# Kernel tuning notes

Hardware: AMD Instinct MI355X
Metric: run time of the kernel (lower is better)

The kernel has to match this reference:

```python
import jax, jax.numpy as jnp
import numpy as np

N = 50000          # nodes
E = 1_600_000      # edges (avg degree 32)
IN_CH = 256
HID = 256          # 2 * out_channels
OUT_CH = 128


def setup_inputs() -> dict:
    key = jax.random.key(0)
    k = jax.random.split(key, 5)
    x = jax.random.normal(k[0], (N, IN_CH), dtype=jnp.float32)
    edge_index = jax.random.randint(k[1], (2, E), 0, N, dtype=jnp.int64)
    W1 = jax.random.normal(k[2], (IN_CH, HID), dtype=jnp.float32) * 0.05
    b1 = jnp.zeros((HID,), dtype=jnp.float32)
    W2 = jax.random.normal(k[3], (HID, OUT_CH), dtype=jnp.float32) * 0.05
    b2 = jnp.zeros((OUT_CH,), dtype=jnp.float32)
    return {"x": x, "edge_index": edge_index, "W1": W1, "b1": b1, "W2": W2, "b2": b2}


def _gcn_conv(x, src, dst, deg_inv_sqrt, W, b, n_nodes):
    # GCNConv: linear transform, then normalized sum-aggregation over edges
    # (edge list already includes self-loops; deg_inv_sqrt precomputed).
    h = x @ W                                   # [N, F_out]
    norm = deg_inv_sqrt[src] * deg_inv_sqrt[dst]  # [E+N]
    msg = h[src] * norm[:, None]                # gather + scale
    out = jax.ops.segment_sum(msg, dst, num_segments=n_nodes)  # scatter-add
    return out + b


def reference(x, edge_index, W1, b1, W2, b2):
    n = x.shape[0]
    loop = jnp.arange(n, dtype=edge_index.dtype)
    src = jnp.concatenate([edge_index[0], loop])   # with self-loops
    dst = jnp.concatenate([edge_index[1], loop])
    # symmetric degree normalization (edge weight 1, deg over targets)
    deg = jax.ops.segment_sum(jnp.ones_like(dst, dtype=x.dtype), dst, num_segments=n)
    deg_inv_sqrt = jnp.where(deg > 0, jax.lax.rsqrt(deg), 0.0)

    z = _gcn_conv(x, src, dst, deg_inv_sqrt, W1, b1, n)
    z = jax.nn.relu(z)
    z = _gcn_conv(z, src, dst, deg_inv_sqrt, W2, b2, n)

    # decode: gather endpoint embeddings of original edges, dot product
    value = jnp.sum(z[edge_index[0]] * z[edge_index[1]], axis=-1)  # [E]
    return value.reshape(-1)
```

## Files before the change

### kernel.cpp

```cpp
#include <hip/hip_runtime.h>

#define WS_ALIGN(x) (((x) + 255) & ~(size_t)255)

typedef float f4v __attribute__((ext_vector_type(4)));
__device__ inline void nt_store4(float* p, float4 v) {
  __builtin_nontemporal_store(*(f4v*)&v, (f4v*)p);
}

__global__ void k_pack_count(const int* __restrict__ src, const int* __restrict__ dst, int E,
                             unsigned int* __restrict__ packed, int* __restrict__ deg) {
  int e = blockIdx.x * blockDim.x + threadIdx.x;
  if (e < E) {
    int s = src[e];
    int d = dst[e];
    packed[e] = (unsigned int)s | ((unsigned int)d << 16);
    atomicAdd(&deg[d], 1);
  }
}

__global__ void k_dis(const int* __restrict__ deg, float* __restrict__ dis, int N) {
  int i = blockIdx.x * blockDim.x + threadIdx.x;
  if (i < N) dis[i] = rsqrtf((float)(deg[i] + 1));
}

__global__ __launch_bounds__(1024) void k_scan(const int* __restrict__ deg,
                                               int* __restrict__ rowptr,
                                               int* __restrict__ cursor,
                                               int N, int Etot) {
  __shared__ int wsum[16];
  __shared__ int s_carry;
  int tid = threadIdx.x, lane = tid & 63, w = tid >> 6;
  if (tid == 0) { s_carry = 0; rowptr[N] = Etot; }
  __syncthreads();
  for (int base = 0; base < N; base += 4096) {
    int i0 = base + tid * 4;
    int v[4];
    #pragma unroll
    for (int u = 0; u < 4; ++u) {
      int i = i0 + u;
      v[u] = (i < N) ? deg[i] : 0;
    }
    int tsum = v[0] + v[1] + v[2] + v[3];
    int sc = tsum;
    #pragma unroll
    for (int off = 1; off < 64; off <<= 1) {
      int t = __shfl_up(sc, off);
      if (lane >= off) sc += t;
    }
    if (lane == 63) wsum[w] = sc;
    __syncthreads();
    if (w == 0 && lane < 16) {
      int xx = wsum[lane];
      #pragma unroll
      for (int off = 1; off < 16; off <<= 1) {
        int t = __shfl_up(xx, off);
        if (lane >= off) xx += t;
      }
      wsum[lane] = xx;
    }
    __syncthreads();
    int woff = (w == 0) ? 0 : wsum[w - 1];
    int excl = s_carry + woff + (sc - tsum);
    #pragma unroll
    for (int u = 0; u < 4; ++u) {
      int i = i0 + u;
      if (i < N) { rowptr[i] = excl; cursor[i] = excl; }
      excl += v[u];
    }
    __syncthreads();
    if (tid == 0) s_carry += wsum[15];
    __syncthreads();
  }
}

__global__ __launch_bounds__(256) void k_fill_xcd(const unsigned int* __restrict__ packed,
                                                  int E, int N,
                                                  int* __restrict__ cursor,
                                                  unsigned short* __restrict__ csr16) {
  int bid = blockIdx.x;
  int xcd = bid & 7;
  int tix = ((bid >> 3) << 8) + threadIdx.x;
  int tpx = ((int)(gridDim.x >> 3)) << 8;
  int lo = (int)(((long long)N * xcd) >> 3);
  int hi = (int)(((long long)N * (xcd + 1)) >> 3);
  for (int e = tix; e < E; e += tpx) {
    unsigned int pk = packed[e];
    int d = (int)(pk >> 16);
    if (d >= lo && d < hi) {
      int pos = atomicAdd(&cursor[d], 1);
      csr16[pos] = (unsigned short)(pk & 0xFFFFu);
    }
  }
}

#define BM 128
#define BN 128
#define BK 16
__global__ __launch_bounds__(256) void k_gemm_scale_sm(const float* __restrict__ A,
                                                       const float* __restrict__ B,
                                                       const float* __restrict__ dis,
                                                       float* __restrict__ C,
                                                       int M, int Nc, int K) {
  __shared__ float As[BK][BM];
  __shared__ float Bs[BK][BN];
  int tid = threadIdx.x;
  int block_row = blockIdx.x * BM;
  int block_col = blockIdx.y * BN;
  int tr = (tid >> 4) << 3;
  int tc = (tid & 15) << 3;
  float acc[8][8] = {};
  for (int k0 = 0; k0 < K; k0 += BK) {
    for (int t = tid; t < BM * BK / 4; t += 256) {
      int r = t >> 2;
      int cc = (t & 3) << 2;
      int gr = block_row + r;
      float4 v = {0.f, 0.f, 0.f, 0.f};
      if (gr < M) v = *(const float4*)(A + (size_t)gr * K + k0 + cc);
      As[cc + 0][r] = v.x; As[cc + 1][r] = v.y; As[cc + 2][r] = v.z; As[cc + 3][r] = v.w;
    }
    for (int t = tid; t < BK * BN / 4; t += 256) {
      int r = t >> 5;
      int cc = (t & 31) << 2;
      *(float4*)&Bs[r][cc] = *(const float4*)(B + (size_t)(k0 + r) * Nc + block_col + cc);
    }
    __syncthreads();
    #pragma unroll
    for (int k = 0; k < BK; ++k) {
      float a[8], b[8];
      *(float4*)&a[0] = *(const float4*)&As[k][tr];
      *(float4*)&a[4] = *(const float4*)&As[k][tr + 4];
      *(float4*)&b[0] = *(const float4*)&Bs[k][tc];
      *(float4*)&b[4] = *(const float4*)&Bs[k][tc + 4];
      #pragma unroll
      for (int i = 0; i < 8; ++i)
        #pragma unroll
        for (int j = 0; j < 8; ++j)
          acc[i][j] = fmaf(a[i], b[j], acc[i][j]);
    }
    __syncthreads();
  }
  int col0 = block_col + tc;
  size_t base = ((size_t)(col0 >> 4) * M) * 16 + (col0 & 15);
  for (int i = 0; i < 8; ++i) {
    int gr = block_row + tr + i;
    if (gr >= M) break;
    float s = dis[gr];
    float4 v0 = {acc[i][0] * s, acc[i][1] * s, acc[i][2] * s, acc[i][3] * s};
    float4 v1 = {acc[i][4] * s, acc[i][5] * s, acc[i][6] * s, acc[i][7] * s};
    float* cp = C + base + (size_t)gr * 16;
    *(float4*)cp = v0;
    *(float4*)(cp + 4) = v1;
  }
}

template <int FCH, bool OUTSLICE>
__global__ __launch_bounds__(256) void k_agg_xcd(const float* __restrict__ hs,
                                                 const int* __restrict__ rowptr,
                                                 const unsigned short* __restrict__ csr,
                                                 const float* __restrict__ dis,
                                                 const float* __restrict__ bias,
                                                 float* __restrict__ out,
                                                 int N, int do_relu, int phase) {
  int bid = blockIdx.x;
  int xcd = bid & 7;
  int wid = threadIdx.x >> 6;
  int lane = threadIdx.x & 63;
  int sub = lane >> 3;
  int epar = (lane >> 2) & 1;
  int c2 = lane & 3;
  int wix = ((bid >> 3) << 2) + wid;
  int wpx = ((int)(gridDim.x >> 3)) << 2;
  int nchunk = (N + 7) >> 3;

  int s = xcd + (phase << 3);
  const float* in = hs + (size_t)s * N * 16;
  for (int ch = wix; ch < nchunk; ch += wpx) {
    int node = (ch << 3) + sub;
    bool valid = node < N;
    int b0 = 0, e0 = 0;
    if (valid) { b0 = rowptr[node]; e0 = rowptr[node + 1]; }
    float4 acc = {0.f, 0.f, 0.f, 0.f};
    int j = b0 + epar;
    for (; j + 6 < e0; j += 8) {
      int i0 = csr[j];     int i1 = csr[j + 2];
      int i2 = csr[j + 4]; int i3 = csr[j + 6];
      float4 v0 = *(const float4*)(in + ((size_t)i0 << 4) + (c2 << 2));
      float4 v1 = *(const float4*)(in + ((size_t)i1 << 4) + (c2 << 2));
      float4 v2 = *(const float4*)(in + ((size_t)i2 << 4) + (c2 << 2));
      float4 v3 = *(const float4*)(in + ((size_t)i3 << 4) + (c2 << 2));
      acc.x += (v0.x + v1.x) + (v2.x + v3.x);
      acc.y += (v0.y + v1.y) + (v2.y + v3.y);
      acc.z += (v0.z + v1.z) + (v2.z + v3.z);
      acc.w += (v0.w + v1.w) + (v2.w + v3.w);
    }
    for (; j < e0; j += 2) {
      int idx = csr[j];
      float4 v = *(const float4*)(in + ((size_t)idx << 4) + (c2 << 2));
      acc.x += v.x; acc.y += v.y; acc.z += v.z; acc.w += v.w;
    }
    acc.x += __shfl_xor(acc.x, 4);
    acc.y += __shfl_xor(acc.y, 4);
    acc.z += __shfl_xor(acc.z, 4);
    acc.w += __shfl_xor(acc.w, 4);
    if (valid && epar == 0) {
      float4 self = *(const float4*)(in + ((size_t)node << 4) + (c2 << 2));
      float dn = dis[node];
      int col = (s << 4) + (c2 << 2);
      float4 bv = *(const float4*)(bias + col);
      float4 r;
      r.x = (acc.x + self.x) * dn + bv.x;
      r.y = (acc.y + self.y) * dn + bv.y;
      r.z = (acc.z + self.z) * dn + bv.z;
      r.w = (acc.w + self.w) * dn + bv.w;
      if (do_relu) {
        r.x = fmaxf(r.x, 0.f); r.y = fmaxf(r.y, 0.f);
        r.z = fmaxf(r.z, 0.f); r.w = fmaxf(r.w, 0.f);
      }
      if (OUTSLICE)
        nt_store4(out + (size_t)s * N * 16 + ((size_t)node << 4) + (c2 << 2), r);
      else
        nt_store4(out + (size_t)node * FCH + col, r);
    }
  }
}

__global__ __launch_bounds__(256) void k_decode_xcd4(const float* __restrict__ z,
                                                     const unsigned int* __restrict__ packed,
                                                     float* __restrict__ partial,
                                                     int E, int N) {
  int bid = blockIdx.x;
  int xcd = bid & 7;
  int wid = threadIdx.x >> 6;
  int lane = threadIdx.x & 63;
  int c2 = lane & 3;
  int sub = lane >> 2;
  int wix = ((bid >> 3) << 2) + wid;
  int wpx = ((int)(gridDim.x >> 3)) << 2;
  const float* zc = z + (size_t)xcd * N * 16;
  float* pp = partial + (size_t)xcd * E;

  for (int e0 = wix * 64; e0 < E; e0 += wpx * 64) {
    float pv[4];
    int ev[4];
    #pragma unroll
    for (int q = 0; q < 4; ++q) {
      int e = e0 + q * 16 + sub;
      ev[q] = e;
      pv[q] = 0.f;
      if (e < E) {
        unsigned int pk = packed[e];
        int a = (int)(pk & 0xFFFFu), d = (int)(pk >> 16);
        float4 za = *(const float4*)(zc + ((size_t)a << 4) + (c2 << 2));
        float4 zb = *(const float4*)(zc + ((size_t)d << 4) + (c2 << 2));
        pv[q] = za.x * zb.x + za.y * zb.y + za.z * zb.z + za.w * zb.w;
      }
    }
    #pragma unroll
    for (int q = 0; q < 4; ++q) {
      pv[q] += __shfl_xor(pv[q], 1);
      pv[q] += __shfl_xor(pv[q], 2);
    }
    if (c2 == 0) {
      #pragma unroll
      for (int q = 0; q < 4; ++q)
        if (ev[q] < E) pp[ev[q]] = pv[q];
    }
  }
}

__global__ void k_dreduce4(const float* __restrict__ partial, float* __restrict__ out, int E) {
  int q = blockIdx.x * 256 + threadIdx.x;
  int e = q << 2;
  if (e >= E) return;
  if (e + 4 <= E) {
    float4 s = *(const float4*)(partial + e);
    #pragma unroll
    for (int k = 1; k < 8; ++k) {
      float4 t = *(const float4*)(partial + (size_t)k * E + e);
      s.x += t.x; s.y += t.y; s.z += t.z; s.w += t.w;
    }
    *(float4*)(out + e) = s;
  } else {
    for (int i = e; i < E; ++i) {
      float s = 0.f;
      #pragma unroll
      for (int k = 0; k < 8; ++k) s += partial[(size_t)k * E + i];
      out[i] = s;
    }
  }
}

extern "C" void kernel_launch(void* const* d_in, const int* in_sizes, int n_in,
                              void* d_out, int out_size, void* d_ws, size_t ws_size,
                              hipStream_t stream) {
  const float* x  = (const float*)d_in[0];
  const int* eidx = (const int*)d_in[1];
  const float* W1 = (const float*)d_in[2];
  const float* b1 = (const float*)d_in[3];
  const float* W2 = (const float*)d_in[4];
  const float* b2 = (const float*)d_in[5];
  float* out = (float*)d_out;

  const int IN_CH = 256, HID = 256, OUT_CH = 128;
  const int N = in_sizes[0] / IN_CH;
  const int E = in_sizes[1] / 2;
  const int* esrc = eidx;
  const int* edst = eidx + E;

  char* p = (char*)d_ws;
  auto alloc = [&](size_t bytes) -> char* { char* r = p; p += WS_ALIGN(bytes); return r; };
  int*   deg    = (int*)  alloc(sizeof(int) * N);
  float* dis    = (float*)alloc(sizeof(float) * N);
  int*   rowptr = (int*)  alloc(sizeof(int) * (N + 1));
  int*   cursor = (int*)  alloc(sizeof(int) * N);
  unsigned short* csr16 = (unsigned short*)alloc(sizeof(unsigned short) * (size_t)E);
  unsigned int*   packed = (unsigned int*) alloc(sizeof(unsigned int) * (size_t)E);
  float* bufA   = (float*)alloc(sizeof(float) * (size_t)N * HID);
  float* bufB   = (float*)alloc(sizeof(float) * (size_t)N * HID);

  const int T = 256;
  const int PG = 2048;

  hipMemsetAsync(deg, 0, sizeof(int) * N, stream);
  hipLaunchKernelGGL(k_pack_count, dim3((E + T - 1) / T), dim3(T), 0, stream,
                     esrc, edst, E, packed, deg);
  hipLaunchKernelGGL(k_dis, dim3((N + T - 1) / T), dim3(T), 0, stream, deg, dis, N);
  hipLaunchKernelGGL(k_scan, dim3(1), dim3(1024), 0, stream, deg, rowptr, cursor, N, E);
  hipLaunchKernelGGL(k_fill_xcd, dim3(PG), dim3(T), 0, stream, packed, E, N, cursor, csr16);

  dim3 g1((N + BM - 1) / BM, HID / BN);
  hipLaunchKernelGGL(k_gemm_scale_sm, g1, dim3(256), 0, stream, x, W1, dis, bufA, N, HID, IN_CH);
  hipLaunchKernelGGL((k_agg_xcd<256, false>), dim3(PG), dim3(256), 0, stream,
                     bufA, rowptr, csr16, dis, b1, bufB, N, 1, 0);
  hipLaunchKernelGGL((k_agg_xcd<256, false>), dim3(PG), dim3(256), 0, stream,
                     bufA, rowptr, csr16, dis, b1, bufB, N, 1, 1);

  dim3 g2((N + BM - 1) / BM, OUT_CH / BN);
  hipLaunchKernelGGL(k_gemm_scale_sm, g2, dim3(256), 0, stream, bufB, W2, dis, bufA, N, OUT_CH, HID);
  hipLaunchKernelGGL((k_agg_xcd<128, true>), dim3(PG), dim3(256), 0, stream,
                     bufA, rowptr, csr16, dis, b2, bufB, N, 0, 0);

  hipLaunchKernelGGL(k_decode_xcd4, dim3(PG), dim3(256), 0, stream,
                     bufB, packed, bufA, E, N);
  hipLaunchKernelGGL(k_dreduce4, dim3((E / 4 + 255) / 256), dim3(256), 0, stream,
                     bufA, out, E);
}
```

Measured before the change: 711.6 us.

## Replace FP32 SIMT GEMM with split-bf16 MFMA GEMM for both layers

Replaces the scalar FMA tiled GEMM with a matrix-core kernel that splits each FP32 operand into high and low bf16 parts and accumulates three bf16 MFMA products (hi*hi, hi*lo, lo*hi) to approximate FP32 precision. Tiles change to 128x64 with four waves, each computing 32x64 using 16x16x32 MFMA instructions. The dis scaling and the sliced output layout are kept. It is meant to cut GEMM compute time, at the cost of conversion work in the load path, scalar strided B loads, scattered scalar stores, and slightly lower precision.

```diff
diff --git a/kernel.cpp b/kernel.cpp
--- a/kernel.cpp
+++ b/kernel.cpp
@@ -3,8 +3,21 @@
 #define WS_ALIGN(x) (((x) + 255) & ~(size_t)255)
 
 typedef float f4v __attribute__((ext_vector_type(4)));
+typedef __attribute__((ext_vector_type(8))) short bf16x8;
+typedef __attribute__((ext_vector_type(4))) float f32x4;
+typedef __attribute__((ext_vector_type(4))) unsigned short us4;
+
 __device__ inline void nt_store4(float* p, float4 v) {
   __builtin_nontemporal_store(*(f4v*)&v, (f4v*)p);
+}
+
+__device__ inline unsigned short f2bf(float v) {
+  unsigned int u = __float_as_uint(v);
+  u += 0x7FFF + ((u >> 16) & 1);
+  return (unsigned short)(u >> 16);
+}
+__device__ inline float bf2f(unsigned short h) {
+  return __uint_as_float(((unsigned int)h) << 16);
 }
 
 __global__ void k_pack_count(const int* __restrict__ src, const int* __restrict__ dst, int E,
@@ -93,63 +106,95 @@
   }
 }
 
-#define BM 128
-#define BN 128
-#define BK 16
-__global__ __launch_bounds__(256) void k_gemm_scale_sm(const float* __restrict__ A,
-                                                       const float* __restrict__ B,
-                                                       const float* __restrict__ dis,
-                                                       float* __restrict__ C,
-                                                       int M, int Nc, int K) {
-  __shared__ float As[BK][BM];
-  __shared__ float Bs[BK][BN];
+#define APAD 40
+__global__ __launch_bounds__(256) void k_gemm_mfma_sm(const float* __restrict__ A,
+                                                      const float* __restrict__ B,
+                                                      const float* __restrict__ dis,
+                                                      float* __restrict__ C,
+                                                      int M, int Nc, int K) {
+  __shared__ unsigned short As_hi[128][APAD];
+  __shared__ unsigned short As_lo[128][APAD];
+  __shared__ unsigned short Bs_hi[64][APAD];
+  __shared__ unsigned short Bs_lo[64][APAD];
   int tid = threadIdx.x;
-  int block_row = blockIdx.x * BM;
-  int block_col = blockIdx.y * BN;
-  int tr = (tid >> 4) << 3;
-  int tc = (tid & 15) << 3;
-  float acc[8][8] = {};
-  for (int k0 = 0; k0 < K; k0 += BK) {
-    for (int t = tid; t < BM * BK / 4; t += 256) {
-      int r = t >> 2;
-      int cc = (t & 3) << 2;
-      int gr = block_row + r;
-      float4 v = {0.f, 0.f, 0.f, 0.f};
-      if (gr < M) v = *(const float4*)(A + (size_t)gr * K + k0 + cc);
-      As[cc + 0][r] = v.x; As[cc + 1][r] = v.y; As[cc + 2][r] = v.z; As[cc + 3][r] = v.w;
-    }
-    for (int t = tid; t < BK * BN / 4; t += 256) {
-      int r = t >> 5;
-      int cc = (t & 31) << 2;
-      *(float4*)&Bs[r][cc] = *(const float4*)(B + (size_t)(k0 + r) * Nc + block_col + cc);
-    }
-    __syncthreads();
-    #pragma unroll
-    for (int k = 0; k < BK; ++k) {
-      float a[8], b[8];
-      *(float4*)&a[0] = *(const float4*)&As[k][tr];
-      *(float4*)&a[4] = *(const float4*)&As[k][tr + 4];
-      *(float4*)&b[0] = *(const float4*)&Bs[k][tc];
-      *(float4*)&b[4] = *(const float4*)&Bs[k][tc + 4];
-      #pragma unroll
-      for (int i = 0; i < 8; ++i)
+  int wv = tid >> 6, lane = tid & 63;
+  int block_row = blockIdx.x * 128;
+  int block_col = blockIdx.y * 64;
+
+  f32x4 acc[2][4] = {};
+
+  for (int k0 = 0; k0 < K; k0 += 32) {
+    {
+      int row = tid >> 1;
+      int grow = block_row + row;
+      int qb = (tid & 1) * 16;
+      const float* ap = A + (size_t)grow * K + k0 + qb;
+      #pragma unroll
+      for (int i = 0; i < 4; ++i) {
+        float4 v = {0.f, 0.f, 0.f, 0.f};
+        if (grow < M) v = *(const float4*)(ap + i * 4);
+        us4 h, l;
+        h.x = f2bf(v.x); h.y = f2bf(v.y); h.z = f2bf(v.z); h.w = f2bf(v.w);
+        l.x = f2bf(v.x - bf2f(h.x)); l.y = f2bf(v.y - bf2f(h.y));
+        l.z = f2bf(v.z - bf2f(h.z)); l.w = f2bf(v.w - bf2f(h.w));
+        *(us4*)&As_hi[row][qb + i * 4] = h;
+        *(us4*)&As_lo[row][qb + i * 4] = l;
+      }
+    }
+    {
+      int n = tid & 63;
+      int ksb = (tid >> 6) * 8;
+      int gn = block_col + n;
+      #pragma unroll
+      for (int j = 0; j < 8; ++j) {
+        float v = B[(size_t)(k0 + ksb + j) * Nc + gn];
+        unsigned short h = f2bf(v);
+        Bs_hi[n][ksb + j] = h;
+        Bs_lo[n][ksb + j] = f2bf(v - bf2f(h));
+      }
+    }
+    __syncthreads();
+    int frow = lane & 15;
+    int fk = (lane >> 4) * 8;
+    bf16x8 ah[2], al[2], bh[4], bl[4];
+    #pragma unroll
+    for (int rf = 0; rf < 2; ++rf) {
+      int r = wv * 32 + rf * 16 + frow;
+      ah[rf] = *(const bf16x8*)&As_hi[r][fk];
+      al[rf] = *(const bf16x8*)&As_lo[r][fk];
+    }
+    #pragma unroll
+    for (int cf = 0; cf < 4; ++cf) {
+      int c = cf * 16 + frow;
+      bh[cf] = *(const bf16x8*)&Bs_hi[c][fk];
+      bl[cf] = *(const bf16x8*)&Bs_lo[c][fk];
+    }
+    #pragma unroll
+    for (int rf = 0; rf < 2; ++rf)
+      #pragma unroll
+      for (int cf = 0; cf < 4; ++cf) {
+        acc[rf][cf] = __builtin_amdgcn_mfma_f32_16x16x32_bf16(ah[rf], bh[cf], acc[rf][cf], 0, 0, 0);
+        acc[rf][cf] = __builtin_amdgcn_mfma_f32_16x16x32_bf16(ah[rf], bl[cf], acc[rf][cf], 0, 0, 0);
+        acc[rf][cf] = __builtin_amdgcn_mfma_f32_16x16x32_bf16(al[rf], bh[cf], acc[rf][cf], 0, 0, 0);
+      }
+    __syncthreads();
+  }
+  int fcol = lane & 15;
+  #pragma unroll
+  for (int rf = 0; rf < 2; ++rf) {
+    int rbase = block_row + wv * 32 + rf * 16 + (lane >> 4) * 4;
+    #pragma unroll
+    for (int j = 0; j < 4; ++j) {
+      int row = rbase + j;
+      if (row < M) {
+        float dn = dis[row];
         #pragma unroll
-        for (int j = 0; j < 8; ++j)
-          acc[i][j] = fmaf(a[i], b[j], acc[i][j]);
-    }
-    __syncthreads();
-  }
-  int col0 = block_col + tc;
-  size_t base = ((size_t)(col0 >> 4) * M) * 16 + (col0 & 15);
-  for (int i = 0; i < 8; ++i) {
-    int gr = block_row + tr + i;
-    if (gr >= M) break;
-    float s = dis[gr];
-    float4 v0 = {acc[i][0] * s, acc[i][1] * s, acc[i][2] * s, acc[i][3] * s};
-    float4 v1 = {acc[i][4] * s, acc[i][5] * s, acc[i][6] * s, acc[i][7] * s};
-    float* cp = C + base + (size_t)gr * 16;
-    *(float4*)cp = v0;
-    *(float4*)(cp + 4) = v1;
+        for (int cf = 0; cf < 4; ++cf) {
+          int sl = (block_col >> 4) + cf;
+          C[((size_t)sl * M + row) * 16 + fcol] = acc[rf][cf][j] * dn;
+        }
+      }
+    }
   }
 }
 
@@ -328,15 +373,15 @@
   hipLaunchKernelGGL(k_scan, dim3(1), dim3(1024), 0, stream, deg, rowptr, cursor, N, E);
   hipLaunchKernelGGL(k_fill_xcd, dim3(PG), dim3(T), 0, stream, packed, E, N, cursor, csr16);
 
-  dim3 g1((N + BM - 1) / BM, HID / BN);
-  hipLaunchKernelGGL(k_gemm_scale_sm, g1, dim3(256), 0, stream, x, W1, dis, bufA, N, HID, IN_CH);
+  dim3 g1((N + 127) / 128, HID / 64);
+  hipLaunchKernelGGL(k_gemm_mfma_sm, g1, dim3(256), 0, stream, x, W1, dis, bufA, N, HID, IN_CH);
   hipLaunchKernelGGL((k_agg_xcd<256, false>), dim3(PG), dim3(256), 0, stream,
                      bufA, rowptr, csr16, dis, b1, bufB, N, 1, 0);
   hipLaunchKernelGGL((k_agg_xcd<256, false>), dim3(PG), dim3(256), 0, stream,
                      bufA, rowptr, csr16, dis, b1, bufB, N, 1, 1);
 
-  dim3 g2((N + BM - 1) / BM, OUT_CH / BN);
-  hipLaunchKernelGGL(k_gemm_scale_sm, g2, dim3(256), 0, stream, bufB, W2, dis, bufA, N, OUT_CH, HID);
+  dim3 g2((N + 127) / 128, OUT_CH / 64);
+  hipLaunchKernelGGL(k_gemm_mfma_sm, g2, dim3(256), 0, stream, bufB, W2, dis, bufA, N, OUT_CH, HID);
   hipLaunchKernelGGL((k_agg_xcd<128, true>), dim3(PG), dim3(256), 0, stream,
                      bufA, rowptr, csr16, dis, b2, bufB, N, 0, 0);
 
```

Measured after the change: 626.6 us, median of 2. 1.14x faster.
